# Optimization experiments

Hardware: AMD Instinct MI355X
Metric: run time of the kernel (lower is better)

The kernel has to match this reference:

```python
import jax, jax.numpy as jnp
import numpy as np

N_ENT, N_REL, E_DIM, R_DIM, K, B = 100000, 64, 128, 128, 32, 16384


def _lookup_maxnorm(table, ids):
    # torch nn.Embedding(max_norm=1): rows with L2 norm > 1 are renormed to 1 at lookup
    x = table[ids]
    n = jnp.linalg.norm(x, axis=-1, keepdims=True)
    return x * jnp.minimum(1.0, 1.0 / jnp.maximum(n, 1e-12))


def setup_inputs() -> dict:
    key = jax.random.key(0)
    ks = jax.random.split(key, 10)
    xavier = lambda k, shp: jax.random.uniform(k, shp, jnp.float32, -1.0, 1.0) * np.sqrt(6.0 / (shp[0] + shp[1]))
    return {
        "idx": jax.random.randint(ks[0], (B,), 0, N_ENT),
        "adj_ent": jax.random.randint(ks[1], (N_ENT, K), 0, N_ENT),
        "adj_rel": jax.random.randint(ks[2], (N_ENT, K), 0, N_REL),
        "ent_table": xavier(ks[3], (N_ENT, E_DIM)),
        "rel_table": xavier(ks[4], (N_REL, R_DIM)),
        "Wr_w": xavier(ks[5], (R_DIM, E_DIM)),
        "Wr_b": jnp.zeros((R_DIM,), jnp.float32),
        "W1_w": xavier(ks[6], (E_DIM, E_DIM)),
        "W1_b": jnp.zeros((E_DIM,), jnp.float32),
        "W2_w": xavier(ks[7], (E_DIM, E_DIM)),
        "W2_b": jnp.zeros((E_DIM,), jnp.float32),
    }


def reference(idx, adj_ent, adj_rel, ent_table, rel_table, Wr_w, Wr_b, W1_w, W1_b, W2_w, W2_b):
    idx = jnp.clip(idx, 0, N_ENT - 1)
    e_ids = adj_ent[idx]                      # [B, K]
    r_ids = adj_rel[idx]                      # [B, K]
    t = _lookup_maxnorm(ent_table, e_ids)     # [B, K, E]
    r = _lookup_maxnorm(rel_table, r_ids)     # [B, K, R]
    h = _lookup_maxnorm(ent_table, idx)       # [B, E]
    # GAT message pass
    hr = h @ Wr_w.T + Wr_b                    # [B, R]
    tr = t @ Wr_w.T + Wr_b                    # [B, K, R]
    score = jnp.sum(jnp.tanh(hr[:, None, :] + r) * tr, axis=-1, keepdims=True)  # [B, K, 1]
    att = jax.nn.softmax(score, axis=1)
    Nh = jnp.sum(t * att, axis=1)             # [B, E]
    # Bi-Interaction aggregate
    leaky = lambda x: jax.nn.leaky_relu(x, 0.2)
    return leaky((h + Nh) @ W1_w.T + W1_b) + leaky((h * Nh) @ W2_w.T + W2_b)
```

## Files before the change

kernel.cpp:

```cpp
#include <hip/hip_runtime.h>
#include <hip/hip_fp16.h>
#include <math.h>

#define N_ENT 100000
#define N_REL 64
#define DIM   128
#define KNB   32
#define BATCH 16384

typedef _Float16 f16;
typedef __attribute__((ext_vector_type(8))) _Float16 f16x8;
typedef __attribute__((ext_vector_type(4))) float floatx4;

__device__ __forceinline__ int clamp_id(int id) {
    return id < 0 ? 0 : (id > N_ENT - 1 ? N_ENT - 1 : id);
}

__device__ __forceinline__ float poly_tanh(float x) {
    const float x2 = x * x;
    return x * fmaf(x2, fmaf(x2, 0.13333334f, -0.33333334f), 1.0f);
}

__global__ __launch_bounds__(256) void k_small(
    const float* __restrict__ Wr, const float* __restrict__ W1,
    const float* __restrict__ W2, f16* __restrict__ Wr16,
    f16* __restrict__ W116, f16* __restrict__ W216,
    const float* __restrict__ rel, __half2* __restrict__ REL2)
{
    if (blockIdx.x < 64) {
        const int t = blockIdx.x * 256 + threadIdx.x;
        Wr16[t] = (f16)Wr[t];
        W116[t] = (f16)W1[t];
        W216[t] = (f16)W2[t];
    } else {
        const int lane = threadIdx.x & 63;
        const int row  = (blockIdx.x - 64) * 4 + (threadIdx.x >> 6);
        const float2 x = *(const float2*)(rel + row * DIM + 2 * lane);
        float ss = x.x * x.x + x.y * x.y;
        #pragma unroll
        for (int m = 1; m < 64; m <<= 1) ss += __shfl_xor(ss, m);
        const float s = fminf(1.0f, 1.0f / fmaxf(sqrtf(ss), 1e-12f));
        REL2[row * 64 + lane] = __floats2half2_rn(x.x * s, x.y * s);
    }
}

__global__ __launch_bounds__(256, 4) void k_pre(
    const float* __restrict__ ent, const f16* __restrict__ B,
    const float* __restrict__ bias, f16* __restrict__ TR16,
    f16* __restrict__ N16)
{
    const int wid  = threadIdx.x >> 6;
    const int lane = threadIdx.x & 63;
    const int strip = blockIdx.x * 4 + wid;
    if (strip >= N_ENT / 16) return;
    const int row0 = strip * 16;
    const int m = lane & 15, quad = lane >> 4;

    const float* __restrict__ src = ent + (size_t)(row0 + m) * DIM + quad * 8;
    float x[4][8];
    #pragma unroll
    for (int kt = 0; kt < 4; ++kt) {
        *(float4*)&x[kt][0] = *(const float4*)(src + kt * 32);
        *(float4*)&x[kt][4] = *(const float4*)(src + kt * 32 + 4);
    }

    float ss = 0.0f;
    #pragma unroll
    for (int kt = 0; kt < 4; ++kt)
        #pragma unroll
        for (int j = 0; j < 8; ++j) ss = fmaf(x[kt][j], x[kt][j], ss);
    ss += __shfl_xor(ss, 16);
    ss += __shfl_xor(ss, 32);
    const float s = fminf(1.0f, 1.0f / fmaxf(sqrtf(ss), 1e-12f));

    f16* __restrict__ ndst = N16 + (size_t)(row0 + m) * DIM + quad * 8;
    f16x8 a[4];
    #pragma unroll
    for (int kt = 0; kt < 4; ++kt) {
        f16x8 av;
        #pragma unroll
        for (int j = 0; j < 8; ++j) av[j] = (f16)(x[kt][j] * s);
        a[kt] = av;
        *(f16x8*)(ndst + kt * 32) = av;
    }

    #pragma unroll
    for (int ct = 0; ct < 8; ++ct) {
        floatx4 acc = {0.0f, 0.0f, 0.0f, 0.0f};
        #pragma unroll
        for (int kt = 0; kt < 4; ++kt) {
            const f16x8 b = *(const f16x8*)(B + (size_t)(ct * 16 + m) * DIM + kt * 32 + quad * 8);
            acc = __builtin_amdgcn_mfma_f32_16x16x32_f16(a[kt], b, acc, 0, 0, 0);
        }
        const float bb = bias[ct * 16 + m];
        #pragma unroll
        for (int r = 0; r < 4; ++r)
            TR16[(size_t)(row0 + quad * 4 + r) * DIM + ct * 16 + m] = (f16)(acc[r] + bb);
    }
}

__global__ __launch_bounds__(256, 4) void k_sa(
    const int* __restrict__ idx, const int* __restrict__ adj_ent,
    const int* __restrict__ adj_rel, const __half2* __restrict__ TR2,
    const __half2* __restrict__ N2, const __half2* __restrict__ REL2,
    __half2* __restrict__ U2, __half2* __restrict__ V2)
{
    const int wid  = threadIdx.x >> 6;
    const int lane = threadIdx.x & 63;
    const int b = blockIdx.x * 4 + wid;

    const int id = clamp_id(idx[b]);
    const float2 hr = __half22float2(TR2[(size_t)id * 64 + lane]);
    const float2 h  = __half22float2(N2[(size_t)id * 64 + lane]);
    const int eL = adj_ent[(size_t)id * KNB + (lane & 31)];
    const int rL = adj_rel[(size_t)id * KNB + (lane & 31)];

    unsigned int tnd[KNB];
    #pragma unroll
    for (int k = 0; k < KNB; ++k) {
        const int e = __builtin_amdgcn_readlane(eL, k);
        tnd[k] = *((const unsigned int*)N2 + (size_t)e * 64 + lane);
    }

    float p[KNB];
    #pragma unroll
    for (int k = 0; k < KNB; ++k) {
        const int e = __builtin_amdgcn_readlane(eL, k);
        const int r = __builtin_amdgcn_readlane(rL, k);
        const float2 tr = __half22float2(TR2[(size_t)e * 64 + lane]);
        const float2 rn = __half22float2(REL2[r * 64 + lane]);
        p[k] = poly_tanh(hr.x + rn.x) * tr.x + poly_tanh(hr.y + rn.y) * tr.y;
    }

    #pragma unroll
    for (int step = 0; step < 5; ++step) {
        const int half = 16 >> step;
        const int mask = 1 << step;
        const bool hi_lane = (lane & mask) != 0;
        #pragma unroll
        for (int i = 0; i < 16; ++i) {
            if (i >= half) break;
            const float lo = p[i], hi = p[i + half];
            const float send = hi_lane ? lo : hi;
            const float recv = __shfl_xor(send, mask);
            p[i] = (hi_lane ? hi : lo) + recv;
        }
    }
    const float sc = p[0] + __shfl_xor(p[0], 32);

    const float ex = __expf(sc);
    float tt = ex;
    #pragma unroll
    for (int m = 1; m < 32; m <<= 1) tt += __shfl_xor(tt, m);
    const float attL = ex * __builtin_amdgcn_rcpf(tt);

    float nh0 = 0.0f, nh1 = 0.0f;
    #pragma unroll
    for (int k = 0; k < KNB; ++k) {
        const float a = __uint_as_float(
            __builtin_amdgcn_readlane(__float_as_uint(attL), k));
        const float2 t = __half22float2(*(const __half2*)&tnd[k]);
        nh0 = fmaf(a, t.x, nh0);
        nh1 = fmaf(a, t.y, nh1);
    }

    U2[(size_t)b * 64 + lane] = __floats2half2_rn(h.x + nh0, h.y + nh1);
    V2[(size_t)b * 64 + lane] = __floats2half2_rn(h.x * nh0, h.y * nh1);
}

__global__ __launch_bounds__(256, 4) void k_gemm_out(
    const f16* __restrict__ U, const f16* __restrict__ V,
    const f16* __restrict__ W1h, const float* __restrict__ b1,
    const f16* __restrict__ W2h, const float* __restrict__ b2,
    float* __restrict__ out)
{
    const int wid  = threadIdx.x >> 6;
    const int lane = threadIdx.x & 63;
    const int g = blockIdx.x * 4 + wid;
    const int strip = g >> 1;
    const int ct0 = (g & 1) * 4;
    const int row0 = strip * 16;
    const int m = lane & 15, quad = lane >> 4;

    f16x8 au[4], av[4];
    #pragma unroll
    for (int kt = 0; kt < 4; ++kt) {
        au[kt] = *(const f16x8*)(U + (size_t)(row0 + m) * DIM + kt * 32 + quad * 8);
        av[kt] = *(const f16x8*)(V + (size_t)(row0 + m) * DIM + kt * 32 + quad * 8);
    }

    #pragma unroll
    for (int c = 0; c < 4; ++c) {
        const int ct = ct0 + c;
        floatx4 accU = {0.0f, 0.0f, 0.0f, 0.0f};
        floatx4 accV = {0.0f, 0.0f, 0.0f, 0.0f};
        #pragma unroll
        for (int kt = 0; kt < 4; ++kt) {
            const f16x8 bu = *(const f16x8*)(W1h + (size_t)(ct * 16 + m) * DIM + kt * 32 + quad * 8);
            const f16x8 bv = *(const f16x8*)(W2h + (size_t)(ct * 16 + m) * DIM + kt * 32 + quad * 8);
            accU = __builtin_amdgcn_mfma_f32_16x16x32_f16(au[kt], bu, accU, 0, 0, 0);
            accV = __builtin_amdgcn_mfma_f32_16x16x32_f16(av[kt], bv, accV, 0, 0, 0);
        }
        const float bb1 = b1[ct * 16 + m];
        const float bb2 = b2[ct * 16 + m];
        #pragma unroll
        for (int r = 0; r < 4; ++r) {
            const float x = accU[r] + bb1;
            const float y = accV[r] + bb2;
            const float lx = x > 0.0f ? x : 0.2f * x;
            const float ly = y > 0.0f ? y : 0.2f * y;
            out[(size_t)(row0 + quad * 4 + r) * DIM + ct * 16 + m] = lx + ly;
        }
    }
}

extern "C" void kernel_launch(void* const* d_in, const int* in_sizes, int n_in,
                              void* d_out, int out_size, void* d_ws, size_t ws_size,
                              hipStream_t stream) {
    (void)in_sizes; (void)n_in; (void)out_size; (void)ws_size;
    const int*   idx     = (const int*)d_in[0];
    const int*   adj_ent = (const int*)d_in[1];
    const int*   adj_rel = (const int*)d_in[2];
    const float* ent     = (const float*)d_in[3];
    const float* rel     = (const float*)d_in[4];
    const float* Wr_w    = (const float*)d_in[5];
    const float* Wr_b    = (const float*)d_in[6];
    const float* W1_w    = (const float*)d_in[7];
    const float* W1_b    = (const float*)d_in[8];
    const float* W2_w    = (const float*)d_in[9];
    const float* W2_b    = (const float*)d_in[10];
    float* out = (float*)d_out;

    char* ws = (char*)d_ws;
    f16* N16   = (f16*)(ws);
    f16* TR16  = (f16*)(ws + 25600000);
    f16* REL16 = (f16*)(ws + 51200000);
    f16* U16   = (f16*)(ws + 51216384);
    f16* V16   = (f16*)(ws + 55410688);
    f16* Wr16  = (f16*)(ws + 59604992);
    f16* W116  = (f16*)(ws + 59637760);
    f16* W216  = (f16*)(ws + 59670528);

    k_small<<<dim3(80), dim3(256), 0, stream>>>(Wr_w, W1_w, W2_w, Wr16, W116, W216,
                                                rel, (__half2*)REL16);
    k_pre<<<dim3((N_ENT / 16 + 3) / 4), dim3(256), 0, stream>>>(ent, Wr16, Wr_b,
                                                                TR16, N16);
    k_sa<<<dim3(BATCH / 4), dim3(256), 0, stream>>>(idx, adj_ent, adj_rel,
                                                    (const __half2*)TR16,
                                                    (const __half2*)N16,
                                                    (const __half2*)REL16,
                                                    (__half2*)U16, (__half2*)V16);
    k_gemm_out<<<dim3(512), dim3(256), 0, stream>>>(U16, V16, W116, W1_b,
                                                    W216, W2_b, out);
}
```

Baseline: 196.9 us.

## Stage Wr in LDS via async loads and process two strips per wave

The k_pre kernel now copies the fp16 Wr weight matrix into shared memory once per block with global_load_lds, instead of every wave re-reading it from global memory. Each wave also handles two 16-row strips, so every B fragment feeds two MFMAs and two ent loads are in flight at once. This cuts redundant weight traffic and raises memory-level parallelism, at the cost of 32KB LDS per block, higher register pressure (which may lower occupancy), and a block-wide barrier. Out-of-range strips are clamped, so the last rows are recomputed rather than skipped.

```diff
diff --git a/kernel.cpp b/kernel.cpp
--- a/kernel.cpp
+++ b/kernel.cpp
@@ -7,6 +7,7 @@
 #define DIM   128
 #define KNB   32
 #define BATCH 16384
+#define STRIPS (N_ENT / 16)
 
 typedef _Float16 f16;
 typedef __attribute__((ext_vector_type(8))) _Float16 f16x8;
@@ -49,53 +50,101 @@
     const float* __restrict__ bias, f16* __restrict__ TR16,
     f16* __restrict__ N16)
 {
+    __shared__ f16 Bs[32 * 512];
     const int wid  = threadIdx.x >> 6;
     const int lane = threadIdx.x & 63;
-    const int strip = blockIdx.x * 4 + wid;
-    if (strip >= N_ENT / 16) return;
-    const int row0 = strip * 16;
     const int m = lane & 15, quad = lane >> 4;
 
-    const float* __restrict__ src = ent + (size_t)(row0 + m) * DIM + quad * 8;
-    float x[4][8];
+    #pragma unroll
+    for (int i = 0; i < 8; ++i) {
+        const int s  = wid * 8 + i;
+        const int ct = s >> 2, kt = s & 3;
+        const f16* gsrc = B + (size_t)(ct * 16 + m) * DIM + kt * 32 + quad * 8;
+        __builtin_amdgcn_global_load_lds(
+            (const __attribute__((address_space(1))) unsigned int*)gsrc,
+            (__attribute__((address_space(3))) unsigned int*)(Bs + s * 512),
+            16, 0, 0);
+    }
+
+    const int wstrip = (blockIdx.x * 4 + wid) * 2;
+    const int s0 = wstrip     < STRIPS ? wstrip     : STRIPS - 1;
+    const int s1 = wstrip + 1 < STRIPS ? wstrip + 1 : STRIPS - 1;
+
+    const float* __restrict__ src0 = ent + (size_t)(s0 * 16 + m) * DIM + quad * 8;
+    const float* __restrict__ src1 = ent + (size_t)(s1 * 16 + m) * DIM + quad * 8;
+    float x0[4][8], x1[4][8];
     #pragma unroll
     for (int kt = 0; kt < 4; ++kt) {
-        *(float4*)&x[kt][0] = *(const float4*)(src + kt * 32);
-        *(float4*)&x[kt][4] = *(const float4*)(src + kt * 32 + 4);
-    }
-
-    float ss = 0.0f;
+        *(float4*)&x0[kt][0] = *(const float4*)(src0 + kt * 32);
+        *(float4*)&x0[kt][4] = *(const float4*)(src0 + kt * 32 + 4);
+    }
+    #pragma unroll
+    for (int kt = 0; kt < 4; ++kt) {
+        *(float4*)&x1[kt][0] = *(const float4*)(src1 + kt * 32);
+        *(float4*)&x1[kt][4] = *(const float4*)(src1 + kt * 32 + 4);
+    }
+    __builtin_amdgcn_sched_barrier(0);
+
+    float ss0 = 0.0f;
     #pragma unroll
     for (int kt = 0; kt < 4; ++kt)
         #pragma unroll
-        for (int j = 0; j < 8; ++j) ss = fmaf(x[kt][j], x[kt][j], ss);
-    ss += __shfl_xor(ss, 16);
-    ss += __shfl_xor(ss, 32);
-    const float s = fminf(1.0f, 1.0f / fmaxf(sqrtf(ss), 1e-12f));
-
-    f16* __restrict__ ndst = N16 + (size_t)(row0 + m) * DIM + quad * 8;
-    f16x8 a[4];
-    #pragma unroll
-    for (int kt = 0; kt < 4; ++kt) {
-        f16x8 av;
-        #pragma unroll
-        for (int j = 0; j < 8; ++j) av[j] = (f16)(x[kt][j] * s);
-        a[kt] = av;
-        *(f16x8*)(ndst + kt * 32) = av;
-    }
+        for (int j = 0; j < 8; ++j) ss0 = fmaf(x0[kt][j], x0[kt][j], ss0);
+    ss0 += __shfl_xor(ss0, 16);
+    ss0 += __shfl_xor(ss0, 32);
+    const float sc0 = fminf(1.0f, 1.0f / fmaxf(sqrtf(ss0), 1e-12f));
+    f16x8 a0[4];
+    {
+        f16* __restrict__ ndst = N16 + (size_t)(s0 * 16 + m) * DIM + quad * 8;
+        #pragma unroll
+        for (int kt = 0; kt < 4; ++kt) {
+            f16x8 av;
+            #pragma unroll
+            for (int j = 0; j < 8; ++j) av[j] = (f16)(x0[kt][j] * sc0);
+            a0[kt] = av;
+            *(f16x8*)(ndst + kt * 32) = av;
+        }
+    }
+
+    float ss1 = 0.0f;
+    #pragma unroll
+    for (int kt = 0; kt < 4; ++kt)
+        #pragma unroll
+        for (int j = 0; j < 8; ++j) ss1 = fmaf(x1[kt][j], x1[kt][j], ss1);
+    ss1 += __shfl_xor(ss1, 16);
+    ss1 += __shfl_xor(ss1, 32);
+    const float sc1 = fminf(1.0f, 1.0f / fmaxf(sqrtf(ss1), 1e-12f));
+    f16x8 a1[4];
+    {
+        f16* __restrict__ ndst = N16 + (size_t)(s1 * 16 + m) * DIM + quad * 8;
+        #pragma unroll
+        for (int kt = 0; kt < 4; ++kt) {
+            f16x8 av;
+            #pragma unroll
+            for (int j = 0; j < 8; ++j) av[j] = (f16)(x1[kt][j] * sc1);
+            a1[kt] = av;
+            *(f16x8*)(ndst + kt * 32) = av;
+        }
+    }
+
+    __syncthreads();
 
     #pragma unroll
     for (int ct = 0; ct < 8; ++ct) {
-        floatx4 acc = {0.0f, 0.0f, 0.0f, 0.0f};
+        floatx4 acc0 = {0.0f, 0.0f, 0.0f, 0.0f};
+        floatx4 acc1 = {0.0f, 0.0f, 0.0f, 0.0f};
         #pragma unroll
         for (int kt = 0; kt < 4; ++kt) {
-            const f16x8 b = *(const f16x8*)(B + (size_t)(ct * 16 + m) * DIM + kt * 32 + quad * 8);
-            acc = __builtin_amdgcn_mfma_f32_16x16x32_f16(a[kt], b, acc, 0, 0, 0);
+            const f16x8 b = *(const f16x8*)(Bs + (ct * 4 + kt) * 512 + lane * 8);
+            acc0 = __builtin_amdgcn_mfma_f32_16x16x32_f16(a0[kt], b, acc0, 0, 0, 0);
+            acc1 = __builtin_amdgcn_mfma_f32_16x16x32_f16(a1[kt], b, acc1, 0, 0, 0);
         }
         const float bb = bias[ct * 16 + m];
         #pragma unroll
-        for (int r = 0; r < 4; ++r)
-            TR16[(size_t)(row0 + quad * 4 + r) * DIM + ct * 16 + m] = (f16)(acc[r] + bb);
+        for (int r = 0; r < 4; ++r) {
+            TR16[(size_t)(s0 * 16 + quad * 4 + r) * DIM + ct * 16 + m] = (f16)(acc0[r] + bb);
+            TR16[(size_t)(s1 * 16 + quad * 4 + r) * DIM + ct * 16 + m] = (f16)(acc1[r] + bb);
+        }
     }
 }
 
@@ -243,8 +292,8 @@
 
     k_small<<<dim3(80), dim3(256), 0, stream>>>(Wr_w, W1_w, W2_w, Wr16, W116, W216,
                                                 rel, (__half2*)REL16);
-    k_pre<<<dim3((N_ENT / 16 + 3) / 4), dim3(256), 0, stream>>>(ent, Wr16, Wr_b,
-                                                                TR16, N16);
+    k_pre<<<dim3((STRIPS + 7) / 8), dim3(256), 0, stream>>>(ent, Wr16, Wr_b,
+                                                            TR16, N16);
     k_sa<<<dim3(BATCH / 4), dim3(256), 0, stream>>>(idx, adj_ent, adj_rel,
                                                     (const __half2*)TR16,
                                                     (const __half2*)N16,
```

Result: faster. 182.1 us (-7.5%).
